# Optimization experiments

Hardware: AMD Instinct MI355X
Metric: run time of the kernel (lower is better)

The kernel has to match this reference:

```python
import jax, jax.numpy as jnp
import numpy as np

N = 50000
E = 500000
IN_F = 128
HEADS = 4
NEG_SLOPE = 0.2


def _gatv2_conv(x, src, dst, Wl, Wr, att, bias, concat):
    # PyG GATv2Conv (share_weights=False): x_l = lin_l(x) for source, x_r = lin_r(x) for target
    n = x.shape[0]
    H, C = att.shape
    xl = (x @ Wl.T).reshape(n, H, C)
    xr = (x @ Wr.T).reshape(n, H, C)
    # per-edge: e_ij = att . leaky_relu(xl[j] + xr[i])
    e = jax.nn.leaky_relu(xl[src] + xr[dst], negative_slope=NEG_SLOPE)  # [E,H,C]
    logit = jnp.einsum('ehc,hc->eh', e, att)  # [E,H]
    # segment softmax over destination node
    lmax = jax.ops.segment_max(logit, dst, num_segments=n)
    lmax = jnp.where(jnp.isfinite(lmax), lmax, 0.0)
    w = jnp.exp(logit - lmax[dst])
    denom = jax.ops.segment_sum(w, dst, num_segments=n)
    alpha = w / (denom[dst] + 1e-16)
    # weighted scatter-aggregate of source messages
    out = jax.ops.segment_sum(xl[src] * alpha[:, :, None], dst, num_segments=n)  # [N,H,C]
    if concat:
        return out.reshape(n, H * C) + bias
    return out.mean(axis=1) + bias


def setup_inputs() -> dict:
    key = jax.random.key(0)
    ks = jax.random.split(key, 11)
    s = 0.1
    x = jax.random.normal(ks[0], (N, IN_F), jnp.float32)
    edge_index = jax.random.randint(ks[1], (2, E), 0, N, dtype=jnp.int32)
    # layer 1: in=128 -> heads=4, C=32, concat -> out 128
    Wl1 = jax.random.normal(ks[2], (128, IN_F), jnp.float32) * s
    Wr1 = jax.random.normal(ks[3], (128, IN_F), jnp.float32) * s
    att1 = jax.random.normal(ks[4], (HEADS, 32), jnp.float32) * s
    b1 = jnp.zeros((128,), jnp.float32)
    # layer 2: in=128 -> heads=4, C=64, mean (concat=False) -> out 64
    Wl2 = jax.random.normal(ks[5], (256, 128), jnp.float32) * s
    Wr2 = jax.random.normal(ks[6], (256, 128), jnp.float32) * s
    att2 = jax.random.normal(ks[7], (HEADS, 64), jnp.float32) * s
    b2 = jnp.zeros((64,), jnp.float32)
    return {"x": x, "edge_index": edge_index, "Wl1": Wl1, "Wr1": Wr1, "att1": att1,
            "b1": b1, "Wl2": Wl2, "Wr2": Wr2, "att2": att2, "b2": b2}


def reference(x, edge_index, Wl1, Wr1, att1, b1, Wl2, Wr2, att2, b2):
    n = x.shape[0]
    loops = jnp.arange(n, dtype=edge_index.dtype)
    src = jnp.concatenate([edge_index[0], loops])  # PyG add_self_loops=True
    dst = jnp.concatenate([edge_index[1], loops])
    # dropout inactive (inference); forward body: elu between layers
    h = jax.nn.elu(_gatv2_conv(x, src, dst, Wl1, Wr1, att1, b1, concat=True))
    logits = _gatv2_conv(h, src, dst, Wl2, Wr2, att2, b2, concat=False)
    return logits
```

## Files before the change

### kernel.cpp

```cpp
#include <hip/hip_runtime.h>
#include <hip/hip_bf16.h>
#include <math.h>


typedef _Float16 half2v __attribute__((ext_vector_type(2)));
typedef _Float16 half4v __attribute__((ext_vector_type(4)));
typedef _Float16 half8v __attribute__((ext_vector_type(8)));
typedef float float4v __attribute__((ext_vector_type(4)));

template <int CTRL>
static __device__ __forceinline__ float dppadd(float x) {
  int y = __builtin_amdgcn_update_dpp(0, __float_as_int(x), CTRL, 0xf, 0xf, true);
  return x + __int_as_float(y);
}

static __device__ __forceinline__ float red8dpp(float p) {
  p = dppadd<0xB1>(p);
  p = dppadd<0x4E>(p);
  p = dppadd<0x141>(p);
  return p;
}


__global__ void cvt_all_kernel(const float* __restrict__ x,
                               const float* __restrict__ wl1, const float* __restrict__ wr1,
                               const float* __restrict__ wl2, const float* __restrict__ wr2,
                               _Float16* __restrict__ xb, _Float16* __restrict__ wb, int n4x) {
  int i = blockIdx.x * blockDim.x + threadIdx.x;
  int stride = gridDim.x * blockDim.x;
  int total = n4x + 24576;
  for (; i < total; i += stride) {
    if (i < n4x) {
      float4 v = ((const float4*)x)[i];
      half4v o = {(_Float16)v.x, (_Float16)v.y, (_Float16)v.z, (_Float16)v.w};
      ((half4v*)xb)[i] = o;
    } else {
      int fj = (i - n4x) * 4;
      const float* src;
      int so;
      if (fj < 16384) { src = wl1; so = fj; }
      else if (fj < 32768) { src = wr1; so = fj - 16384; }
      else if (fj < 65536) { src = wl2; so = fj - 32768; }
      else { src = wr2; so = fj - 65536; }
      float4 v = *(const float4*)(src + so);
      half4v o = {(_Float16)v.x, (_Float16)v.y, (_Float16)v.z, (_Float16)v.w};
      *(half4v*)(wb + fj) = o;
    }
  }
}


__global__ void count_kernel(const int* __restrict__ dst, int* __restrict__ deg, int E) {
  int i = blockIdx.x * blockDim.x + threadIdx.x;
  if (i < E) atomicAdd(&deg[dst[i]], 1);
}

__global__ void partial_kernel(const int* __restrict__ deg, int* __restrict__ partial, int N) {
  int t = threadIdx.x;
  int i = blockIdx.x * 256 + t;
  int v = (i < N) ? deg[i] : 0;
  v += __shfl_xor(v, 1); v += __shfl_xor(v, 2); v += __shfl_xor(v, 4);
  v += __shfl_xor(v, 8); v += __shfl_xor(v, 16); v += __shfl_xor(v, 32);
  __shared__ int ws[4];
  if ((t & 63) == 0) ws[t >> 6] = v;
  __syncthreads();
  if (t == 0) partial[blockIdx.x] = ws[0] + ws[1] + ws[2] + ws[3];
}

__global__ void scan_partials_kernel(int* __restrict__ partial, int nb) {
  __shared__ int s[256];
  int t = threadIdx.x;
  int v = (t < nb) ? partial[t] : 0;
  s[t] = v;
  __syncthreads();
  for (int off = 1; off < 256; off <<= 1) {
    int u = (t >= off) ? s[t - off] : 0;
    __syncthreads();
    s[t] += u;
    __syncthreads();
  }
  if (t < nb) partial[t] = s[t] - v;
}

__global__ void scan_final_kernel(const int* __restrict__ deg, const int* __restrict__ partial,
                                  int* __restrict__ row_ptr, int* __restrict__ cursor,
                                  int N, int E) {
  __shared__ int s[256];
  int t = threadIdx.x;
  int i = blockIdx.x * 256 + t;
  int v = (i < N) ? deg[i] : 0;
  s[t] = v;
  __syncthreads();
  for (int off = 1; off < 256; off <<= 1) {
    int u = (t >= off) ? s[t - off] : 0;
    __syncthreads();
    s[t] += u;
    __syncthreads();
  }
  int excl = s[t] - v + partial[blockIdx.x];
  if (i < N) {
    row_ptr[i] = excl;
    cursor[i] = excl;
  }
  if (blockIdx.x == 0 && t == 0) row_ptr[N] = E;
}

__global__ void fill_kernel(const int* __restrict__ src, const int* __restrict__ dst,
                            int* __restrict__ cursor, int* __restrict__ col, int E) {
  int i = blockIdx.x * blockDim.x + threadIdx.x;
  if (i < E) {
    int d = dst[i];
    int pos = atomicAdd(&cursor[d], 1);
    col[pos] = src[i];
  }
}

__global__ __launch_bounds__(256) void gemm_mfma2(
    const _Float16* __restrict__ A, const _Float16* __restrict__ Wa,
    const _Float16* __restrict__ Wb, _Float16* __restrict__ Ca,
    _Float16* __restrict__ Cb, int N, int Oa, int ldC) {
  __shared__ _Float16 lds[32768];
  int t = threadIdx.x;
  int gbase = blockIdx.y * 256;
#pragma unroll
  for (int i = 0; i < 16; ++i) {
    int c = t + i * 256;
    int row = c >> 4, kc = c & 15;
    int grow = gbase + row;
    const _Float16* srcW =
        (grow < Oa) ? (Wa + (size_t)grow * 128) : (Wb + (size_t)(grow - Oa) * 128);
    half8v v = *(const half8v*)(srcW + kc * 8);
    int off16 = (row << 4) | (kc ^ (row & 7));
    *(half8v*)((char*)lds + (off16 << 4)) = v;
  }
  __syncthreads();
  int wv = t >> 6, lane = t & 63;
  int l15 = lane & 15, l4 = lane >> 4;
  int row0 = blockIdx.x * 64 + (wv & 1) * 32;
  int colw = (wv >> 1) * 128;
  int gc = gbase + colw;
  half8v xf[2][4];
#pragma unroll
  for (int rg = 0; rg < 2; ++rg) {
    int r = row0 + rg * 16 + l15;
    bool valid = r < N;
    const half8v* Ar = (const half8v*)(A + (size_t)r * 128 + l4 * 8);
#pragma unroll
    for (int kk = 0; kk < 4; ++kk) {
      half8v z = {};
      xf[rg][kk] = valid ? Ar[kk * 4] : z;
    }
  }
  int wrow = colw + l15;
  float4v acc[2][8] = {};
#pragma unroll
  for (int kk = 0; kk < 4; ++kk) {
    int xorterm = ((kk * 4 + l4) ^ (l15 & 7)) << 4;
    const char* base = (const char*)lds + wrow * 256 + xorterm;
    half8v wf[8];
#pragma unroll
    for (int ot = 0; ot < 8; ++ot) wf[ot] = *(const half8v*)(base + ot * 4096);
#pragma unroll
    for (int ot = 0; ot < 8; ++ot) {
      acc[0][ot] = __builtin_amdgcn_mfma_f32_16x16x32_f16(wf[ot], xf[0][kk], acc[0][ot], 0, 0, 0);
      acc[1][ot] = __builtin_amdgcn_mfma_f32_16x16x32_f16(wf[ot], xf[1][kk], acc[1][ot], 0, 0, 0);
    }
  }
  bool isA = gc < Oa;
  _Float16* C = isA ? Ca : Cb;
  int cb = isA ? gc : gc - Oa;
#pragma unroll
  for (int rg = 0; rg < 2; ++rg) {
    int r = row0 + rg * 16 + l15;
    if (r < N) {
#pragma unroll
      for (int ot = 0; ot < 8; ++ot) {
        half4v o = {(_Float16)acc[rg][ot][0], (_Float16)acc[rg][ot][1],
                    (_Float16)acc[rg][ot][2], (_Float16)acc[rg][ot][3]};
        *(half4v*)(C + (size_t)r * ldC + cb + ot * 16 + l4 * 4) = o;
      }
    }
  }
}


__global__ __launch_bounds__(256) void agg1_kernel(
    const _Float16* __restrict__ xl, const _Float16* __restrict__ xr,
    const float* __restrict__ att, const float* __restrict__ bias,
    const int* __restrict__ row_ptr, const int* __restrict__ col,
    _Float16* __restrict__ hout, int N) {
  int wid = (blockIdx.x * blockDim.x + threadIdx.x) >> 6;
  int lane = threadIdx.x & 63;
  if (wid >= N) return;
  int eslot = lane >> 5, sub = lane & 31;
  const int d0 = sub * 4;
  const _Float16* xld = xl + d0;
  half4v xrv = *(const half4v*)(xr + (size_t)wid * 128 + d0);
  float4 atf = *(const float4*)(att + d0);
  half2v atlo = {(_Float16)atf.x, (_Float16)atf.y};
  half2v athi = {(_Float16)atf.z, (_Float16)atf.w};
  half4v k4 = {(_Float16)0.2f, (_Float16)0.2f, (_Float16)0.2f, (_Float16)0.2f};
  int e0 = row_ptr[wid];
  int deg = row_ptr[wid + 1] - e0;
  float s, a0, a1, a2, a3;
  {
    half4v v = *(const half4v*)(xld + (size_t)wid * 128);
    half4v u = v + xrv;
    half4v lr = __builtin_elementwise_max(u, u * k4);
    float p = __builtin_amdgcn_fdot2((half2v){lr.x, lr.y}, atlo, 0.f, false);
    p = __builtin_amdgcn_fdot2((half2v){lr.z, lr.w}, athi, p, false);
    p = red8dpp(p);
    float w = (eslot == 0) ? __expf(p) : 0.f;
    s = w;
    a0 = w * (float)v.x; a1 = w * (float)v.y; a2 = w * (float)v.z; a3 = w * (float)v.w;
  }
  int niter = (deg + 1) >> 1;
  if (niter > 0) {
    int idx = eslot;
    bool valid = idx < deg;
    int srcn = col[e0 + (valid ? idx : 0)];
    half4v vcur = *(const half4v*)(xld + (size_t)srcn * 128);
    for (int j = 0; j < niter; ++j) {
      int nidx = idx + 2;
      bool nvalid = nidx < deg;
      int nsrc = col[e0 + (nvalid ? nidx : 0)];
      half4v vnxt = *(const half4v*)(xld + (size_t)nsrc * 128);
      half4v u = vcur + xrv;
      half4v lr = __builtin_elementwise_max(u, u * k4);
      float p = __builtin_amdgcn_fdot2((half2v){lr.x, lr.y}, atlo, 0.f, false);
      p = __builtin_amdgcn_fdot2((half2v){lr.z, lr.w}, athi, p, false);
      p = red8dpp(p);
      float w = valid ? __expf(p) : 0.f;
      s += w;
      a0 = fmaf(w, (float)vcur.x, a0);
      a1 = fmaf(w, (float)vcur.y, a1);
      a2 = fmaf(w, (float)vcur.z, a2);
      a3 = fmaf(w, (float)vcur.w, a3);
      vcur = vnxt; idx = nidx; valid = nvalid;
    }
  }
  s += __shfl_xor(s, 32);
  a0 += __shfl_xor(a0, 32); a1 += __shfl_xor(a1, 32);
  a2 += __shfl_xor(a2, 32); a3 += __shfl_xor(a3, 32);
  float inv = 1.f / (s + 1e-16f);
  float4 bi = *(const float4*)(bias + d0);
  float o0 = a0 * inv + bi.x, o1 = a1 * inv + bi.y;
  float o2 = a2 * inv + bi.z, o3 = a3 * inv + bi.w;
  o0 = o0 > 0.f ? o0 : __expf(o0) - 1.f;
  o1 = o1 > 0.f ? o1 : __expf(o1) - 1.f;
  o2 = o2 > 0.f ? o2 : __expf(o2) - 1.f;
  o3 = o3 > 0.f ? o3 : __expf(o3) - 1.f;
  if (eslot == 0) {
    half4v o = {(_Float16)o0, (_Float16)o1, (_Float16)o2, (_Float16)o3};
    *(half4v*)(hout + (size_t)wid * 128 + d0) = o;
  }
}

__global__ __launch_bounds__(256) void agg2_kernel(
    const _Float16* __restrict__ xl, const _Float16* __restrict__ xr,
    const float* __restrict__ att, const float* __restrict__ bias,
    const int* __restrict__ row_ptr, const int* __restrict__ col,
    float* __restrict__ out, int N) {
  int wid = (blockIdx.x * blockDim.x + threadIdx.x) >> 6;
  int lane = threadIdx.x & 63;
  if (wid >= N) return;
  int eslot = lane >> 5, sub = lane & 31;
  const int d0 = sub * 8;
  const _Float16* xld = xl + d0;
  half8v xrv = *(const half8v*)(xr + (size_t)wid * 256 + d0);
  float4 af0 = *(const float4*)(att + d0);
  float4 af1 = *(const float4*)(att + d0 + 4);
  half2v at[4] = {{(_Float16)af0.x, (_Float16)af0.y}, {(_Float16)af0.z, (_Float16)af0.w},
                  {(_Float16)af1.x, (_Float16)af1.y}, {(_Float16)af1.z, (_Float16)af1.w}};
  half8v k8 = {(_Float16)0.2f, (_Float16)0.2f, (_Float16)0.2f, (_Float16)0.2f,
               (_Float16)0.2f, (_Float16)0.2f, (_Float16)0.2f, (_Float16)0.2f};
  int e0 = row_ptr[wid];
  int deg = row_ptr[wid + 1] - e0;
  float s, ac[8];
  {
    half8v v = *(const half8v*)(xld + (size_t)wid * 256);
    half8v u = v + xrv;
    half8v lr = __builtin_elementwise_max(u, u * k8);
    float p = __builtin_amdgcn_fdot2((half2v){lr[0], lr[1]}, at[0], 0.f, false);
    p = __builtin_amdgcn_fdot2((half2v){lr[2], lr[3]}, at[1], p, false);
    p = __builtin_amdgcn_fdot2((half2v){lr[4], lr[5]}, at[2], p, false);
    p = __builtin_amdgcn_fdot2((half2v){lr[6], lr[7]}, at[3], p, false);
    p = red8dpp(p);
    float w = (eslot == 0) ? __expf(p) : 0.f;
    s = w;
#pragma unroll
    for (int k = 0; k < 8; ++k) ac[k] = w * (float)v[k];
  }
  int niter = (deg + 1) >> 1;
  if (niter > 0) {
    int idx = eslot;
    bool valid = idx < deg;
    int srcn = col[e0 + (valid ? idx : 0)];
    half8v vcur = *(const half8v*)(xld + (size_t)srcn * 256);
    for (int j = 0; j < niter; ++j) {
      int nidx = idx + 2;
      bool nvalid = nidx < deg;
      int nsrc = col[e0 + (nvalid ? nidx : 0)];
      half8v vnxt = *(const half8v*)(xld + (size_t)nsrc * 256);
      half8v u = vcur + xrv;
      half8v lr = __builtin_elementwise_max(u, u * k8);
      float p = __builtin_amdgcn_fdot2((half2v){lr[0], lr[1]}, at[0], 0.f, false);
      p = __builtin_amdgcn_fdot2((half2v){lr[2], lr[3]}, at[1], p, false);
      p = __builtin_amdgcn_fdot2((half2v){lr[4], lr[5]}, at[2], p, false);
      p = __builtin_amdgcn_fdot2((half2v){lr[6], lr[7]}, at[3], p, false);
      p = red8dpp(p);
      float w = valid ? __expf(p) : 0.f;
      s += w;
#pragma unroll
      for (int k = 0; k < 8; ++k) ac[k] = fmaf(w, (float)vcur[k], ac[k]);
      vcur = vnxt; idx = nidx; valid = nvalid;
    }
  }
  s += __shfl_xor(s, 32);
#pragma unroll
  for (int k = 0; k < 8; ++k) ac[k] += __shfl_xor(ac[k], 32);
  float inv = 1.f / (s + 1e-16f);
#pragma unroll
  for (int k = 0; k < 8; ++k) ac[k] *= inv;
#pragma unroll
  for (int k = 0; k < 8; ++k) {
    ac[k] += __shfl_xor(ac[k], 8);
    ac[k] += __shfl_xor(ac[k], 16);
  }
  if (lane < 8) {
    float4 b0 = *(const float4*)(bias + lane * 8);
    float4 b1v = *(const float4*)(bias + lane * 8 + 4);
    float4 o0 = make_float4(ac[0] * 0.25f + b0.x, ac[1] * 0.25f + b0.y,
                            ac[2] * 0.25f + b0.z, ac[3] * 0.25f + b0.w);
    float4 o1 = make_float4(ac[4] * 0.25f + b1v.x, ac[5] * 0.25f + b1v.y,
                            ac[6] * 0.25f + b1v.z, ac[7] * 0.25f + b1v.w);
    float* op = out + (size_t)wid * 64 + lane * 8;
    *(float4*)op = o0;
    *(float4*)(op + 4) = o1;
  }
}

extern "C" void kernel_launch(void* const* d_in, const int* in_sizes, int n_in,
                              void* d_out, int out_size, void* d_ws, size_t ws_size,
                              hipStream_t stream) {
  const float* x = (const float*)d_in[0];
  const int* ei = (const int*)d_in[1];
  const float* Wl1 = (const float*)d_in[2];
  const float* Wr1 = (const float*)d_in[3];
  const float* att1 = (const float*)d_in[4];
  const float* b1 = (const float*)d_in[5];
  const float* Wl2 = (const float*)d_in[6];
  const float* Wr2 = (const float*)d_in[7];
  const float* att2 = (const float*)d_in[8];
  const float* b2 = (const float*)d_in[9];
  float* out = (float*)d_out;

  int N = in_sizes[0] / 128;
  int E = in_sizes[1] / 2;
  const int* srcArr = ei;
  const int* dstArr = ei + E;

  char* w = (char*)d_ws;
  auto alloc = [&](size_t bytes) {
    char* p = w;
    w += (bytes + 255) & ~(size_t)255;
    return p;
  };
  int* row_ptr = (int*)alloc((size_t)(N + 1) * sizeof(int));
  int* cursor = (int*)alloc((size_t)N * sizeof(int));
  int* partial = (int*)alloc(256 * sizeof(int));
  int* col = (int*)alloc((size_t)E * sizeof(int));
  _Float16* xb = (_Float16*)alloc((size_t)N * 128 * 2);
  _Float16* wb = (_Float16*)alloc(98304 * 2);
  _Float16* hb = (_Float16*)alloc((size_t)N * 128 * 2);
  _Float16* xl1 = (_Float16*)alloc((size_t)N * 128 * 2);
  _Float16* xr1 = (_Float16*)alloc((size_t)N * 128 * 2);
  _Float16* xl2 = (_Float16*)alloc((size_t)N * 256 * 2);
  _Float16* xr2 = (_Float16*)alloc((size_t)N * 256 * 2);

  const _Float16* wl1b = wb;
  const _Float16* wr1b = wb + 16384;
  const _Float16* wl2b = wb + 32768;
  const _Float16* wr2b = wb + 65536;

  cvt_all_kernel<<<1024, 256, 0, stream>>>(x, Wl1, Wr1, Wl2, Wr2, xb, wb, N * 32);

  hipMemsetAsync(cursor, 0, (size_t)N * sizeof(int), stream);
  count_kernel<<<(E + 255) / 256, 256, 0, stream>>>(dstArr, cursor, E);
  int nb = (N + 255) / 256;
  partial_kernel<<<nb, 256, 0, stream>>>(cursor, partial, N);
  scan_partials_kernel<<<1, 256, 0, stream>>>(partial, nb);
  scan_final_kernel<<<nb, 256, 0, stream>>>(cursor, partial, row_ptr, cursor, N, E);
  fill_kernel<<<(E + 255) / 256, 256, 0, stream>>>(srcArr, dstArr, cursor, col, E);

  int gx = (N + 63) / 64;
  gemm_mfma2<<<dim3(gx, 1), 256, 0, stream>>>(xb, wl1b, wr1b, xl1, xr1, N, 128, 128);
  agg1_kernel<<<(N * 64 + 255) / 256, 256, 0, stream>>>(xl1, xr1, att1, b1, row_ptr, col, hb, N);

  gemm_mfma2<<<dim3(gx, 2), 256, 0, stream>>>(hb, wl2b, wr2b, xl2, xr2, N, 256, 256);
  agg2_kernel<<<(N * 64 + 255) / 256, 256, 0, stream>>>(xl2, xr2, att2, b2, row_ptr, col, out, N);
}
```

Before: 202.7 us.

## Fuse conversion with degree count, merge scans, deepen gather prefetch in aggregation

Folds the degree-count atomics into the fp16 conversion kernel and merges the partial-sum scan into the final scan kernel, cutting two launches. The aggregation kernels now prefetch two edges ahead with clamped indices, drop the per-edge validity predicate (odd tail handled separately), and fold log2(e) into the attention vector so exp2f replaces __expf. They also use 32-bit shift/or indexing and 128-thread blocks. Every scan block now redundantly rescans the partials array, and the fp16 rounding of the scaled attention weights differs slightly from before.

```diff
diff --git a/kernel.cpp b/kernel.cpp
--- a/kernel.cpp
+++ b/kernel.cpp
@@ -22,19 +22,21 @@
 }
 
 
-__global__ void cvt_all_kernel(const float* __restrict__ x,
-                               const float* __restrict__ wl1, const float* __restrict__ wr1,
-                               const float* __restrict__ wl2, const float* __restrict__ wr2,
-                               _Float16* __restrict__ xb, _Float16* __restrict__ wb, int n4x) {
+__global__ void fused_cvt_count_kernel(
+    const float* __restrict__ x,
+    const float* __restrict__ wl1, const float* __restrict__ wr1,
+    const float* __restrict__ wl2, const float* __restrict__ wr2,
+    _Float16* __restrict__ xb, _Float16* __restrict__ wb,
+    const int* __restrict__ dst, int* __restrict__ deg, int n4x, int E) {
   int i = blockIdx.x * blockDim.x + threadIdx.x;
   int stride = gridDim.x * blockDim.x;
-  int total = n4x + 24576;
+  int total = n4x + 24576 + E;
   for (; i < total; i += stride) {
     if (i < n4x) {
       float4 v = ((const float4*)x)[i];
       half4v o = {(_Float16)v.x, (_Float16)v.y, (_Float16)v.z, (_Float16)v.w};
       ((half4v*)xb)[i] = o;
-    } else {
+    } else if (i < n4x + 24576) {
       int fj = (i - n4x) * 4;
       const float* src;
       int so;
@@ -45,15 +47,12 @@
       float4 v = *(const float4*)(src + so);
       half4v o = {(_Float16)v.x, (_Float16)v.y, (_Float16)v.z, (_Float16)v.w};
       *(half4v*)(wb + fj) = o;
-    }
-  }
-}
-
-
-__global__ void count_kernel(const int* __restrict__ dst, int* __restrict__ deg, int E) {
-  int i = blockIdx.x * blockDim.x + threadIdx.x;
-  if (i < E) atomicAdd(&deg[dst[i]], 1);
-}
+    } else {
+      atomicAdd(&deg[dst[i - n4x - 24576]], 1);
+    }
+  }
+}
+
 
 __global__ void partial_kernel(const int* __restrict__ deg, int* __restrict__ partial, int N) {
   int t = threadIdx.x;
@@ -67,26 +66,22 @@
   if (t == 0) partial[blockIdx.x] = ws[0] + ws[1] + ws[2] + ws[3];
 }
 
-__global__ void scan_partials_kernel(int* __restrict__ partial, int nb) {
+__global__ void scan_final_kernel(const int* __restrict__ deg, const int* __restrict__ partial,
+                                  int* __restrict__ row_ptr, int* __restrict__ cursor,
+                                  int N, int E, int nb) {
+  __shared__ int sp[256];
   __shared__ int s[256];
   int t = threadIdx.x;
-  int v = (t < nb) ? partial[t] : 0;
-  s[t] = v;
+  int pv = (t < nb) ? partial[t] : 0;
+  sp[t] = pv;
   __syncthreads();
   for (int off = 1; off < 256; off <<= 1) {
-    int u = (t >= off) ? s[t - off] : 0;
+    int u = (t >= off) ? sp[t - off] : 0;
     __syncthreads();
-    s[t] += u;
+    sp[t] += u;
     __syncthreads();
   }
-  if (t < nb) partial[t] = s[t] - v;
-}
-
-__global__ void scan_final_kernel(const int* __restrict__ deg, const int* __restrict__ partial,
-                                  int* __restrict__ row_ptr, int* __restrict__ cursor,
-                                  int N, int E) {
-  __shared__ int s[256];
-  int t = threadIdx.x;
+  int blockpre = (blockIdx.x > 0) ? sp[blockIdx.x - 1] : 0;
   int i = blockIdx.x * 256 + t;
   int v = (i < N) ? deg[i] : 0;
   s[t] = v;
@@ -97,7 +92,7 @@
     s[t] += u;
     __syncthreads();
   }
-  int excl = s[t] - v + partial[blockIdx.x];
+  int excl = s[t] - v + blockpre;
   if (i < N) {
     row_ptr[i] = excl;
     cursor[i] = excl;
@@ -184,7 +179,7 @@
 }
 
 
-__global__ __launch_bounds__(256) void agg1_kernel(
+__global__ __launch_bounds__(128) void agg1_kernel(
     const _Float16* __restrict__ xl, const _Float16* __restrict__ xr,
     const float* __restrict__ att, const float* __restrict__ bias,
     const int* __restrict__ row_ptr, const int* __restrict__ col,
@@ -193,50 +188,64 @@
   int lane = threadIdx.x & 63;
   if (wid >= N) return;
   int eslot = lane >> 5, sub = lane & 31;
-  const int d0 = sub * 4;
-  const _Float16* xld = xl + d0;
-  half4v xrv = *(const half4v*)(xr + (size_t)wid * 128 + d0);
+  const uint d0 = (uint)sub * 4u;
+  const float L2E = 1.44269504f;
+  half4v xrv = *(const half4v*)(xr + (((uint)wid << 7) | d0));
   float4 atf = *(const float4*)(att + d0);
-  half2v atlo = {(_Float16)atf.x, (_Float16)atf.y};
-  half2v athi = {(_Float16)atf.z, (_Float16)atf.w};
+  half2v atlo = {(_Float16)(atf.x * L2E), (_Float16)(atf.y * L2E)};
+  half2v athi = {(_Float16)(atf.z * L2E), (_Float16)(atf.w * L2E)};
   half4v k4 = {(_Float16)0.2f, (_Float16)0.2f, (_Float16)0.2f, (_Float16)0.2f};
   int e0 = row_ptr[wid];
   int deg = row_ptr[wid + 1] - e0;
+  const int* ecol = col + e0;
   float s, a0, a1, a2, a3;
   {
-    half4v v = *(const half4v*)(xld + (size_t)wid * 128);
+    half4v v = *(const half4v*)(xl + (((uint)wid << 7) | d0));
     half4v u = v + xrv;
     half4v lr = __builtin_elementwise_max(u, u * k4);
     float p = __builtin_amdgcn_fdot2((half2v){lr.x, lr.y}, atlo, 0.f, false);
     p = __builtin_amdgcn_fdot2((half2v){lr.z, lr.w}, athi, p, false);
     p = red8dpp(p);
-    float w = (eslot == 0) ? __expf(p) : 0.f;
+    float w = (eslot == 0) ? exp2f(p) : 0.f;
     s = w;
     a0 = w * (float)v.x; a1 = w * (float)v.y; a2 = w * (float)v.z; a3 = w * (float)v.w;
   }
-  int niter = (deg + 1) >> 1;
-  if (niter > 0) {
+  if (deg > 0) {
+    int dm1 = deg - 1;
     int idx = eslot;
-    bool valid = idx < deg;
-    int srcn = col[e0 + (valid ? idx : 0)];
-    half4v vcur = *(const half4v*)(xld + (size_t)srcn * 128);
-    for (int j = 0; j < niter; ++j) {
-      int nidx = idx + 2;
-      bool nvalid = nidx < deg;
-      int nsrc = col[e0 + (nvalid ? nidx : 0)];
-      half4v vnxt = *(const half4v*)(xld + (size_t)nsrc * 128);
-      half4v u = vcur + xrv;
+    int cA = ecol[min(idx, dm1)];
+    int cB = ecol[min(idx + 2, dm1)];
+    half4v vA = *(const half4v*)(xl + (((uint)cA << 7) | d0));
+    half4v vB = *(const half4v*)(xl + (((uint)cB << 7) | d0));
+    int M = deg >> 1;
+    for (int j = 0; j < M; ++j) {
+      int cC = ecol[min(idx + 4, dm1)];
+      half4v vC = *(const half4v*)(xl + (((uint)cC << 7) | d0));
+      half4v u = vA + xrv;
       half4v lr = __builtin_elementwise_max(u, u * k4);
       float p = __builtin_amdgcn_fdot2((half2v){lr.x, lr.y}, atlo, 0.f, false);
       p = __builtin_amdgcn_fdot2((half2v){lr.z, lr.w}, athi, p, false);
       p = red8dpp(p);
-      float w = valid ? __expf(p) : 0.f;
+      float w = exp2f(p);
       s += w;
-      a0 = fmaf(w, (float)vcur.x, a0);
-      a1 = fmaf(w, (float)vcur.y, a1);
-      a2 = fmaf(w, (float)vcur.z, a2);
-      a3 = fmaf(w, (float)vcur.w, a3);
-      vcur = vnxt; idx = nidx; valid = nvalid;
+      a0 = fmaf(w, (float)vA.x, a0);
+      a1 = fmaf(w, (float)vA.y, a1);
+      a2 = fmaf(w, (float)vA.z, a2);
+      a3 = fmaf(w, (float)vA.w, a3);
+      vA = vB; vB = vC; idx += 2;
+    }
+    if (deg & 1) {
+      half4v u = vA + xrv;
+      half4v lr = __builtin_elementwise_max(u, u * k4);
+      float p = __builtin_amdgcn_fdot2((half2v){lr.x, lr.y}, atlo, 0.f, false);
+      p = __builtin_amdgcn_fdot2((half2v){lr.z, lr.w}, athi, p, false);
+      p = red8dpp(p);
+      float w = (eslot == 0) ? exp2f(p) : 0.f;
+      s += w;
+      a0 = fmaf(w, (float)vA.x, a0);
+      a1 = fmaf(w, (float)vA.y, a1);
+      a2 = fmaf(w, (float)vA.z, a2);
+      a3 = fmaf(w, (float)vA.w, a3);
     }
   }
   s += __shfl_xor(s, 32);
@@ -252,11 +261,11 @@
   o3 = o3 > 0.f ? o3 : __expf(o3) - 1.f;
   if (eslot == 0) {
     half4v o = {(_Float16)o0, (_Float16)o1, (_Float16)o2, (_Float16)o3};
-    *(half4v*)(hout + (size_t)wid * 128 + d0) = o;
-  }
-}
-
-__global__ __launch_bounds__(256) void agg2_kernel(
+    *(half4v*)(hout + (((uint)wid << 7) | d0)) = o;
+  }
+}
+
+__global__ __launch_bounds__(128) void agg2_kernel(
     const _Float16* __restrict__ xl, const _Float16* __restrict__ xr,
     const float* __restrict__ att, const float* __restrict__ bias,
     const int* __restrict__ row_ptr, const int* __restrict__ col,
@@ -265,20 +274,23 @@
   int lane = threadIdx.x & 63;
   if (wid >= N) return;
   int eslot = lane >> 5, sub = lane & 31;
-  const int d0 = sub * 8;
-  const _Float16* xld = xl + d0;
-  half8v xrv = *(const half8v*)(xr + (size_t)wid * 256 + d0);
+  const uint d0 = (uint)sub * 8u;
+  const float L2E = 1.44269504f;
+  half8v xrv = *(const half8v*)(xr + (((uint)wid << 8) | d0));
   float4 af0 = *(const float4*)(att + d0);
   float4 af1 = *(const float4*)(att + d0 + 4);
-  half2v at[4] = {{(_Float16)af0.x, (_Float16)af0.y}, {(_Float16)af0.z, (_Float16)af0.w},
-                  {(_Float16)af1.x, (_Float16)af1.y}, {(_Float16)af1.z, (_Float16)af1.w}};
+  half2v at[4] = {{(_Float16)(af0.x * L2E), (_Float16)(af0.y * L2E)},
+                  {(_Float16)(af0.z * L2E), (_Float16)(af0.w * L2E)},
+                  {(_Float16)(af1.x * L2E), (_Float16)(af1.y * L2E)},
+                  {(_Float16)(af1.z * L2E), (_Float16)(af1.w * L2E)}};
   half8v k8 = {(_Float16)0.2f, (_Float16)0.2f, (_Float16)0.2f, (_Float16)0.2f,
                (_Float16)0.2f, (_Float16)0.2f, (_Float16)0.2f, (_Float16)0.2f};
   int e0 = row_ptr[wid];
   int deg = row_ptr[wid + 1] - e0;
+  const int* ecol = col + e0;
   float s, ac[8];
   {
-    half8v v = *(const half8v*)(xld + (size_t)wid * 256);
+    half8v v = *(const half8v*)(xl + (((uint)wid << 8) | d0));
     half8v u = v + xrv;
     half8v lr = __builtin_elementwise_max(u, u * k8);
     float p = __builtin_amdgcn_fdot2((half2v){lr[0], lr[1]}, at[0], 0.f, false);
@@ -286,34 +298,47 @@
     p = __builtin_amdgcn_fdot2((half2v){lr[4], lr[5]}, at[2], p, false);
     p = __builtin_amdgcn_fdot2((half2v){lr[6], lr[7]}, at[3], p, false);
     p = red8dpp(p);
-    float w = (eslot == 0) ? __expf(p) : 0.f;
+    float w = (eslot == 0) ? exp2f(p) : 0.f;
     s = w;
 #pragma unroll
     for (int k = 0; k < 8; ++k) ac[k] = w * (float)v[k];
   }
-  int niter = (deg + 1) >> 1;
-  if (niter > 0) {
+  if (deg > 0) {
+    int dm1 = deg - 1;
     int idx = eslot;
-    bool valid = idx < deg;
-    int srcn = col[e0 + (valid ? idx : 0)];
-    half8v vcur = *(const half8v*)(xld + (size_t)srcn * 256);
-    for (int j = 0; j < niter; ++j) {
-      int nidx = idx + 2;
-      bool nvalid = nidx < deg;
-      int nsrc = col[e0 + (nvalid ? nidx : 0)];
-      half8v vnxt = *(const half8v*)(xld + (size_t)nsrc * 256);
-      half8v u = vcur + xrv;
+    int cA = ecol[min(idx, dm1)];
+    int cB = ecol[min(idx + 2, dm1)];
+    half8v vA = *(const half8v*)(xl + (((uint)cA << 8) | d0));
+    half8v vB = *(const half8v*)(xl + (((uint)cB << 8) | d0));
+    int M = deg >> 1;
+    for (int j = 0; j < M; ++j) {
+      int cC = ecol[min(idx + 4, dm1)];
+      half8v vC = *(const half8v*)(xl + (((uint)cC << 8) | d0));
+      half8v u = vA + xrv;
       half8v lr = __builtin_elementwise_max(u, u * k8);
       float p = __builtin_amdgcn_fdot2((half2v){lr[0], lr[1]}, at[0], 0.f, false);
       p = __builtin_amdgcn_fdot2((half2v){lr[2], lr[3]}, at[1], p, false);
       p = __builtin_amdgcn_fdot2((half2v){lr[4], lr[5]}, at[2], p, false);
       p = __builtin_amdgcn_fdot2((half2v){lr[6], lr[7]}, at[3], p, false);
       p = red8dpp(p);
-      float w = valid ? __expf(p) : 0.f;
+      float w = exp2f(p);
       s += w;
 #pragma unroll
-      for (int k = 0; k < 8; ++k) ac[k] = fmaf(w, (float)vcur[k], ac[k]);
-      vcur = vnxt; idx = nidx; valid = nvalid;
+      for (int k = 0; k < 8; ++k) ac[k] = fmaf(w, (float)vA[k], ac[k]);
+      vA = vB; vB = vC; idx += 2;
+    }
+    if (deg & 1) {
+      half8v u = vA + xrv;
+      half8v lr = __builtin_elementwise_max(u, u * k8);
+      float p = __builtin_amdgcn_fdot2((half2v){lr[0], lr[1]}, at[0], 0.f, false);
+      p = __builtin_amdgcn_fdot2((half2v){lr[2], lr[3]}, at[1], p, false);
+      p = __builtin_amdgcn_fdot2((half2v){lr[4], lr[5]}, at[2], p, false);
+      p = __builtin_amdgcn_fdot2((half2v){lr[6], lr[7]}, at[3], p, false);
+      p = red8dpp(p);
+      float w = (eslot == 0) ? exp2f(p) : 0.f;
+      s += w;
+#pragma unroll
+      for (int k = 0; k < 8; ++k) ac[k] = fmaf(w, (float)vA[k], ac[k]);
     }
   }
   s += __shfl_xor(s, 32);
@@ -383,20 +408,20 @@
   const _Float16* wl2b = wb + 32768;
   const _Float16* wr2b = wb + 65536;
 
-  cvt_all_kernel<<<1024, 256, 0, stream>>>(x, Wl1, Wr1, Wl2, Wr2, xb, wb, N * 32);
-
   hipMemsetAsync(cursor, 0, (size_t)N * sizeof(int), stream);
-  count_kernel<<<(E + 255) / 256, 256, 0, stream>>>(dstArr, cursor, E);
+  fused_cvt_count_kernel<<<2048, 256, 0, stream>>>(x, Wl1, Wr1, Wl2, Wr2, xb, wb,
+                                                   dstArr, cursor, N * 32, E);
+
   int nb = (N + 255) / 256;
   partial_kernel<<<nb, 256, 0, stream>>>(cursor, partial, N);
-  scan_partials_kernel<<<1, 256, 0, stream>>>(partial, nb);
-  scan_final_kernel<<<nb, 256, 0, stream>>>(cursor, partial, row_ptr, cursor, N, E);
+  scan_final_kernel<<<nb, 256, 0, stream>>>(cursor, partial, row_ptr, cursor, N, E, nb);
   fill_kernel<<<(E + 255) / 256, 256, 0, stream>>>(srcArr, dstArr, cursor, col, E);
 
   int gx = (N + 63) / 64;
+  int aggBlocks = (N * 64 + 127) / 128;
   gemm_mfma2<<<dim3(gx, 1), 256, 0, stream>>>(xb, wl1b, wr1b, xl1, xr1, N, 128, 128);
-  agg1_kernel<<<(N * 64 + 255) / 256, 256, 0, stream>>>(xl1, xr1, att1, b1, row_ptr, col, hb, N);
+  agg1_kernel<<<aggBlocks, 128, 0, stream>>>(xl1, xr1, att1, b1, row_ptr, col, hb, N);
 
   gemm_mfma2<<<dim3(gx, 2), 256, 0, stream>>>(hb, wl2b, wr2b, xl2, xr2, N, 256, 256);
-  agg2_kernel<<<(N * 64 + 255) / 256, 256, 0, stream>>>(xl2, xr2, att2, b2, row_ptr, col, out, N);
-}
+  agg2_kernel<<<aggBlocks, 128, 0, stream>>>(xl2, xr2, att2, b2, row_ptr, col, out, N);
+}
```

Measured after the change: 190.7 us. -5.9%, faster.
